# Kernel tuning notes

Measured on AMD Instinct MI355X. Metric: run time of the kernel, lower is better.

## Reference

```python
import jax, jax.numpy as jnp
import numpy as np

DIM, HEADS, WS = 256, 16, 8
B, H, W = 2, 252, 252
BN_EPS = 1e-5


def _rel_index():
    # Same construction as the torch buffer relative_position_index (64,64)
    coords = np.stack(np.meshgrid(np.arange(WS), np.arange(WS), indexing='ij'))
    flat = coords.reshape(2, -1)
    rel = (flat[:, :, None] - flat[:, None, :]).transpose(1, 2, 0).copy()
    rel[..., 0] += WS - 1
    rel[..., 1] += WS - 1
    rel[..., 0] *= 2 * WS - 1
    return jnp.asarray(rel.sum(-1))

REL_IDX = _rel_index()  # (WS*WS, WS*WS) int


def _conv(x, w, pad, groups=1):
    return jax.lax.conv_general_dilated(
        x, w, (1, 1), [(pad[0], pad[0]), (pad[1], pad[1])],
        dimension_numbers=('NCHW', 'OIHW', 'NCHW'), feature_group_count=groups)


def setup_inputs() -> dict:
    key = jax.random.key(0)
    ks = jax.random.split(key, 8)
    s = lambda k, shape, sc: jax.random.normal(k, shape, jnp.float32) * sc
    z = lambda: jnp.zeros((DIM,), jnp.float32)
    return {
        'x': s(ks[0], (B, DIM, H, W), 1.0),
        'w_qkv': s(ks[1], (3 * DIM, DIM, 1, 1), 0.05),
        'rel_bias_table': s(ks[2], ((2 * WS - 1) ** 2, HEADS), 0.02),
        'w_h': s(ks[3], (DIM, DIM, WS, 1), 0.02),
        'b_h': z(),
        'w_v': s(ks[4], (DIM, DIM, 1, WS), 0.02),
        'b_v': z(),
        'w_dw': s(ks[5], (DIM, 1, WS, WS), 0.05),
        'bn_gamma': jnp.ones((DIM,), jnp.float32),
        'bn_beta': z(),
        'bn_mean': z(),
        'bn_var': jnp.ones((DIM,), jnp.float32),
        'w_pw': s(ks[6], (DIM, DIM, 1, 1), 0.05),
    }


def reference(x, w_qkv, rel_bias_table, w_h, b_h, w_v, b_v, w_dw,
              bn_gamma, bn_beta, bn_mean, bn_var, w_pw):
    Bc, C, Hc, Wc = x.shape
    pad_h, pad_w = WS - Hc % WS, WS - Wc % WS
    xp = jnp.pad(x, ((0, 0), (0, 0), (0, pad_h), (0, pad_w)), mode='reflect')
    Hp, Wp = Hc + pad_h, Wc + pad_w
    hh, ww, d = Hp // WS, Wp // WS, C // HEADS

    qkv = _conv(xp, w_qkv, (0, 0))  # (B, 3C, Hp, Wp)
    # b (qkv h d) (hh ws1) (ww ws2) -> qkv (b hh ww) h (ws1 ws2) d
    qkv = qkv.reshape(Bc, 3, HEADS, d, hh, WS, ww, WS)
    qkv = qkv.transpose(1, 0, 4, 6, 2, 5, 7, 3).reshape(3, Bc * hh * ww, HEADS, WS * WS, d)
    q, k, v = qkv[0], qkv[1], qkv[2]

    dots = jnp.einsum('nhid,nhjd->nhij', q, k) * (d ** -0.5)
    bias = rel_bias_table[REL_IDX.reshape(-1)].reshape(WS * WS, WS * WS, HEADS)
    dots = dots + bias.transpose(2, 0, 1)[None]  # (1, h, 64, 64)
    attn = jax.nn.softmax(dots, axis=-1)
    out = jnp.einsum('nhij,nhjd->nhid', attn, v)
    # (b hh ww) h (ws1 ws2) d -> b (h d) (hh ws1) (ww ws2)
    out = out.reshape(Bc, hh, ww, HEADS, WS, WS, d)
    out = out.transpose(0, 3, 6, 1, 4, 2, 5).reshape(Bc, C, Hp, Wp)
    out = out[:, :, :Hc, :Wc]

    p1 = _conv(jnp.pad(out, ((0, 0), (0, 0), (0, 1), (0, 0)), mode='reflect'),
               w_h, (WS // 2 - 1, 0)) + b_h[None, :, None, None]
    p2 = _conv(jnp.pad(out, ((0, 0), (0, 0), (0, 0), (0, 1)), mode='reflect'),
               w_v, (0, WS // 2 - 1)) + b_v[None, :, None, None]
    y = jnp.pad(p1 + p2, ((0, 0), (0, 0), (0, 1), (0, 1)), mode='reflect')
    y = _conv(y, w_dw, ((WS - 1) // 2, (WS - 1) // 2), groups=DIM)  # depthwise
    inv = bn_gamma / jnp.sqrt(bn_var + BN_EPS)
    y = y * inv[None, :, None, None] + (bn_beta - bn_mean * inv)[None, :, None, None]
    y = _conv(y, w_pw, (0, 0))  # pointwise 1x1
    return y[:, :, :Hc, :Wc]
```

## Files before the change

### kernel.cpp

```cpp
#include <hip/hip_runtime.h>
#include <hip/hip_bf16.h>

#define HC 252
#define WC 252
#define CD 256
#define NHEADS 16

#define XP_W 264
#define XP_HW (252*264)
#define XP_CHW (256*252*264)

typedef unsigned short u16;
typedef unsigned int u32;
typedef __attribute__((ext_vector_type(8))) short bf16x8;
typedef __attribute__((ext_vector_type(4))) float f32x4;
typedef __attribute__((ext_vector_type(4))) u32 u32x4;
typedef __attribute__((ext_vector_type(2))) u32 u32x2;

#define XP_BYTES (2u * (unsigned)XP_CHW * 2u)
#define ZP_OFF   XP_BYTES
#define ZP_BYTES 409600u
#define WT_OFF   (ZP_OFF + ZP_BYTES)
#define WT_ELEMS (128*8192)
#define WPW_OFF  (WT_OFF + (unsigned)WT_ELEMS*2u)
#define WPW_ELEMS (8*8192)
#define WQ_OFF   (WPW_OFF + (unsigned)WPW_ELEMS*2u)
#define WQ_ELEMS (768*256)
#define BIAS_OFF (WQ_OFF + (unsigned)WQ_ELEMS*2u)

__device__ __forceinline__ u16 bfu(float f) {
    __hip_bfloat16 h = __float2bfloat16(f);
    return *(reinterpret_cast<u16*>(&h));
}
__device__ __forceinline__ u32 pack2(float a, float b) {
    return (u32)bfu(a) | ((u32)bfu(b) << 16);
}

__global__ __launch_bounds__(256, 2) void attn_mfma(
    const float* __restrict__ x, const u16* __restrict__ WQ,
    const float* __restrict__ BIASF, u16* __restrict__ xp)
{
    __shared__ __align__(16) char smem[73728];

    const int bid = blockIdx.x;
    const int zz = (bid & 7) * 256 + (bid >> 3);
    const int wx = zz & 31, wy = (zz >> 5) & 31, b = zz >> 10;
    const int tid = threadIdx.x;
    const int lane = tid & 63, wid = tid >> 6;
    const int g = lane >> 4, li = lane & 15;

    {
        int ci = tid;
        const float* srcc = x + (size_t)(b * 256 + ci) * (HC * WC);
        #pragma unroll
        for (int r = 0; r < 8; ++r) {
            int h = wy * 8 + r; if (h >= HC) h = 2 * HC - 2 - h;
            const float* src = srcc + h * WC;
            float v[8];
            if (wx == 31) {
                #pragma unroll
                for (int c = 0; c < 8; ++c) {
                    int w = 248 + c; if (w >= WC) w = 2 * WC - 2 - w;
                    v[c] = src[w];
                }
            } else {
                float4 f0 = *(const float4*)(src + wx * 8);
                float4 f1 = *(const float4*)(src + wx * 8 + 4);
                v[0]=f0.x; v[1]=f0.y; v[2]=f0.z; v[3]=f0.w;
                v[4]=f1.x; v[5]=f1.y; v[6]=f1.z; v[7]=f1.w;
            }
            #pragma unroll
            for (int c = 0; c < 8; ++c) {
                int pos = r * 8 + c;
                int byte = pos * 512 + ((ci * 2) ^ ((pos & 7) << 4));
                *(u16*)(smem + byte) = bfu(v[c]);
            }
        }
    }
    __syncthreads();

    const int WB = 32768 + wid * 10240;
    char* Qb = smem + WB;
    char* Kb = smem + WB + 2048;
    char* Vb = smem + WB + 4096;
    char* Pb = smem + WB + 6144;

    const bf16x8 zf = {0,0,0,0,0,0,0,0};

    #pragma unroll 1
    for (int hh = 0; hh < 4; ++hh) {
        const int head = wid * 4 + hh;

        f32x4 acc[3][4];
        #pragma unroll
        for (int p = 0; p < 3; ++p)
            #pragma unroll
            for (int nf = 0; nf < 4; ++nf) acc[p][nf] = (f32x4){0.f,0.f,0.f,0.f};

        for (int ks = 0; ks < 8; ++ks) {
            bf16x8 bx[4];
            #pragma unroll
            for (int nf = 0; nf < 4; ++nf) {
                int pos = 16 * nf + li;
                int byte = pos * 512 + ((ks * 64 + 16 * g) ^ ((pos & 7) << 4));
                bx[nf] = *(const bf16x8*)(smem + byte);
            }
            bf16x8 aw[3];
            #pragma unroll
            for (int p = 0; p < 3; ++p) {
                int o = p * 256 + head * 16 + li;
                aw[p] = *(const bf16x8*)(WQ + o * 256 + ks * 32 + 8 * g);
            }
            __builtin_amdgcn_s_setprio(1);
            #pragma unroll
            for (int p = 0; p < 3; ++p)
                #pragma unroll
                for (int nf = 0; nf < 4; ++nf)
                    acc[p][nf] = __builtin_amdgcn_mfma_f32_16x16x32_bf16(aw[p], bx[nf], acc[p][nf], 0, 0, 0);
            __builtin_amdgcn_s_setprio(0);
        }

        #pragma unroll
        for (int p = 0; p < 3; ++p) {
            if (p < 2) {
                char* base = (p == 0) ? Qb : Kb;
                #pragma unroll
                for (int nf = 0; nf < 4; ++nf) {
                    int pos = 16 * nf + li;
                    u32 lo = pack2(acc[p][nf][0], acc[p][nf][1]);
                    u32 hi = pack2(acc[p][nf][2], acc[p][nf][3]);
                    int byte = pos * 32 + ((8 * g) ^ (((pos >> 2) & 1) << 4));
                    *(u32x2*)(base + byte) = (u32x2){lo, hi};
                }
            } else {
                #pragma unroll
                for (int nf = 0; nf < 4; ++nf) {
                    int pos = 16 * nf + li;
                    #pragma unroll
                    for (int r = 0; r < 4; ++r) {
                        int d = 4 * g + r;
                        int byte = (pos >> 3) * 256 + d * 16 + (pos & 7) * 2;
                        *(u16*)(Vb + byte) = bfu(acc[p][nf][r]);
                    }
                }
            }
        }

        f32x4 s[4][4];
        #pragma unroll
        for (int mf = 0; mf < 4; ++mf)
            #pragma unroll
            for (int nf = 0; nf < 4; ++nf) s[mf][nf] = (f32x4){0.f,0.f,0.f,0.f};
        bf16x8 bk[4];
        #pragma unroll
        for (int nf = 0; nf < 4; ++nf) {
            int pos = 16 * nf + li;
            bk[nf] = (g < 2) ? *(const bf16x8*)(Kb + pos * 32 + ((16 * g) ^ (((pos >> 2) & 1) << 4))) : zf;
        }
        __builtin_amdgcn_s_setprio(1);
        #pragma unroll
        for (int mf = 0; mf < 4; ++mf) {
            int pos = 16 * mf + li;
            bf16x8 aq = (g < 2) ? *(const bf16x8*)(Qb + pos * 32 + ((16 * g) ^ (((pos >> 2) & 1) << 4))) : zf;
            #pragma unroll
            for (int nf = 0; nf < 4; ++nf)
                s[mf][nf] = __builtin_amdgcn_mfma_f32_16x16x32_bf16(aq, bk[nf], s[mf][nf], 0, 0, 0);
        }
        __builtin_amdgcn_s_setprio(0);

        f32x4 e[4][4];
        f32x4 rs[4];
        #pragma unroll
        for (int mf = 0; mf < 4; ++mf) rs[mf] = (f32x4){0.f,0.f,0.f,0.f};
        #pragma unroll
        for (int mf = 0; mf < 4; ++mf)
            #pragma unroll
            for (int nf = 0; nf < 4; ++nf) {
                f32x4 b4 = *(const f32x4*)(BIASF + (((head * 4 + mf) * 4 + nf) * 64 + lane) * 4);
                #pragma unroll
                for (int r = 0; r < 4; ++r) {
                    float ev = __expf(s[mf][nf][r] * 0.25f + b4[r]);
                    e[mf][nf][r] = ev;
                    rs[mf][r] += ev;
                }
            }
        #pragma unroll
        for (int mf = 0; mf < 4; ++mf)
            #pragma unroll
            for (int r = 0; r < 4; ++r) {
                float t = rs[mf][r];
                t += __shfl_xor(t, 1); t += __shfl_xor(t, 2);
                t += __shfl_xor(t, 4); t += __shfl_xor(t, 8);
                rs[mf][r] = t;
            }

        f32x4 o[4];
        #pragma unroll
        for (int mf = 0; mf < 4; ++mf) o[mf] = (f32x4){0.f,0.f,0.f,0.f};
        const bool even = !(lane & 1);
        #pragma unroll
        for (int hf = 0; hf < 2; ++hf) {
            #pragma unroll
            for (int mf = 0; mf < 4; ++mf)
                #pragma unroll
                for (int nfl = 0; nfl < 2; ++nfl) {
                    f32x4 ee = e[mf][2 * hf + nfl];
                    float p0 = __shfl_xor(ee[0], 1), p1 = __shfl_xor(ee[1], 1);
                    float p2 = __shfl_xor(ee[2], 1), p3 = __shfl_xor(ee[3], 1);
                    int jl = 16 * nfl + (li & ~1);
                    u32 w0, w1; int r0;
                    if (even) { w0 = pack2(ee[0], p0); w1 = pack2(ee[1], p1); r0 = 0; }
                    else      { w0 = pack2(p2, ee[2]); w1 = pack2(p3, ee[3]); r0 = 2; }
                    int i0 = 16 * mf + 4 * g + r0, i1 = i0 + 1;
                    *(u32*)(Pb + i0 * 64 + ((2 * jl) ^ ((i0 & 3) << 4))) = w0;
                    *(u32*)(Pb + i1 * 64 + ((2 * jl) ^ ((i1 & 3) << 4))) = w1;
                }
            bf16x8 bv = *(const bf16x8*)(Vb + (4 * hf + g) * 256 + li * 16);
            __builtin_amdgcn_s_setprio(1);
            #pragma unroll
            for (int mf = 0; mf < 4; ++mf) {
                int i = 16 * mf + li;
                bf16x8 ap = *(const bf16x8*)(Pb + i * 64 + ((16 * g) ^ ((i & 3) << 4)));
                o[mf] = __builtin_amdgcn_mfma_f32_16x16x32_bf16(ap, bv, o[mf], 0, 0, 0);
            }
            __builtin_amdgcn_s_setprio(0);
        }

        #pragma unroll
        for (int mf = 0; mf < 4; ++mf) {
            int h = wy * 8 + 2 * mf + (g >> 1);
            int wbase = wx * 8 + 4 * (g & 1);
            if (h < HC && wbase < WC) {
                float v0 = o[mf][0] / rs[mf][0], v1 = o[mf][1] / rs[mf][1];
                float v2 = o[mf][2] / rs[mf][2], v3 = o[mf][3] / rs[mf][3];
                size_t idx = ((size_t)(b * 256 + head * 16 + li) * HC + h) * XP_W + wbase + 4;
                *(u32x2*)(xp + idx) = (u32x2){pack2(v0, v1), pack2(v2, v3)};
            }
        }
    }
}

__global__ __launch_bounds__(256) void wprep_kernel(
    const float* __restrict__ wh, const float* __restrict__ wv,
    const float* __restrict__ wpw, const float* __restrict__ wqkv,
    const float* __restrict__ btab, u16* __restrict__ wsu)
{
    int i = blockIdx.x * 256 + threadIdx.x;
    u16* WT = wsu + WT_OFF / 2;
    u16* WP = wsu + WPW_OFF / 2;
    u16* ZP = wsu + ZP_OFF / 2;
    u16* WQp = wsu + WQ_OFF / 2;
    float* BF = (float*)(wsu + BIAS_OFF / 2);
    if (i < WT_ELEMS) {
        int j = i & 7, co = (i >> 3) & 255, kb = (i >> 11) & 3, s = i >> 13;
        float v = (s < 64) ? wh[co * 2048 + s * 32 + kb * 8 + j]
                           : wv[co * 2048 + (s - 64) * 32 + kb * 8 + j];
        WT[i] = bfu(v);
    } else if (i < WT_ELEMS + WPW_ELEMS) {
        int i2 = i - WT_ELEMS;
        int j = i2 & 7, co = (i2 >> 3) & 255, kb = (i2 >> 11) & 3, s = i2 >> 13;
        WP[i2] = bfu(wpw[co * 256 + s * 32 + kb * 8 + j]);
    } else if (i < WT_ELEMS + WPW_ELEMS + (int)(ZP_BYTES / 2)) {
        ZP[i - WT_ELEMS - WPW_ELEMS] = 0;
    } else if (i < WT_ELEMS + WPW_ELEMS + (int)(ZP_BYTES / 2) + WQ_ELEMS) {
        int i4 = i - WT_ELEMS - WPW_ELEMS - (int)(ZP_BYTES / 2);
        WQp[i4] = bfu(wqkv[i4]);
    } else {
        int i5 = i - WT_ELEMS - WPW_ELEMS - (int)(ZP_BYTES / 2) - WQ_ELEMS;
        if (i5 < 16384) {
            int lane = i5 & 63, nf = (i5 >> 6) & 3, mf = (i5 >> 8) & 3, head = i5 >> 10;
            int gg = lane >> 4, ll = lane & 15;
            #pragma unroll
            for (int r = 0; r < 4; ++r) {
                int row = 16 * mf + 4 * gg + r;
                int col = 16 * nf + ll;
                int dy = (row >> 3) - (col >> 3) + 7;
                int dx = (row & 7) - (col & 7) + 7;
                BF[i5 * 4 + r] = btab[(dy * 15 + dx) * NHEADS + head];
            }
        }
    }
}

__global__ __launch_bounds__(256) void halo_kernel(u16* __restrict__ xp)
{
    int i = blockIdx.x * 256 + threadIdx.x;
    if (i >= 129024 * 12) return;
    int row = i / 12, c = i % 12;
    int wp = (c < 4) ? c : 252 + c;
    u16 v = 0;
    if (wp == 256) v = xp[row * XP_W + 254];
    xp[row * XP_W + wp] = v;
}

__global__ __launch_bounds__(512, 2) void sepconv_mfma(
    const u16* __restrict__ xp, const u16* __restrict__ WT,
    const u16* __restrict__ ZP,
    const float* __restrict__ b_h, const float* __restrict__ b_v,
    float* __restrict__ P)
{
    __shared__ u16 As[2][8192];
    __shared__ u16 Bs[2][256 * 36];

    const int bid = blockIdx.x;
    const int zz = (bid & 7) * 63 + (bid >> 3);
    const int h = zz % HC, b = zz / HC;
    const int tid = threadIdx.x;
    const int lane = tid & 63, wid = tid >> 6;
    const int wr = wid >> 2, wc = wid & 3;
    const int cq = lane & 15, kb = lane >> 4;

    const int wl2 = (tid & 127) * 2;
    const int oc = tid >> 7;

    const u16* hcur[8];
    int hstep[8];
    #pragma unroll
    for (int t = 0; t < 8; ++t) {
        int j = h + t - 3;
        bool valid = (j >= 0 && j <= 252);
        int jr = (j == 252) ? 250 : j;
        hcur[t] = valid ? (xp + (size_t)b * XP_CHW + (size_t)jr * XP_W) : ZP;
        hstep[t] = valid ? 4 * XP_HW : 0;
    }
    const u16* vbase = xp + (size_t)b * XP_CHW + (size_t)h * XP_W;
    const int hvoff = oc * XP_HW + wl2 + 4;

    const int bw0 = wl2 * 36 + oc * 8;
    const int bw1 = bw0 + 36;

    f32x4 acc[8][4];
    #pragma unroll
    for (int m = 0; m < 8; ++m)
        #pragma unroll
        for (int n = 0; n < 4; ++n) acc[m][n] = (f32x4){0.f, 0.f, 0.f, 0.f};

    u32x4 rA[2];
    u32 rB[8];

    int aw0, aw1;
    {
        int c0 = tid, c1 = 512 + tid;
        aw0 = ((c0 >> 8) * 256 + ((c0 & 255) ^ (((c0 >> 8) & 3) << 1))) * 8;
        aw1 = ((c1 >> 8) * 256 + ((c1 & 255) ^ (((c1 >> 8) & 3) << 1))) * 8;
    }

    rA[0] = *(const u32x4*)(WT + (size_t)tid * 8);
    rA[1] = *(const u32x4*)(WT + (size_t)(512 + tid) * 8);
    #pragma unroll
    for (int t = 0; t < 8; ++t)
        rB[t] = *(const u32*)(hcur[t] + hvoff);
    *(u32x4*)&As[0][aw0] = rA[0];
    *(u32x4*)&As[0][aw1] = rA[1];
    {
        union { bf16x8 v; u32 u[4]; } p0, p1;
        #pragma unroll
        for (int q = 0; q < 4; ++q) {
            p0.u[q] = __builtin_amdgcn_perm(rB[2 * q + 1], rB[2 * q], 0x05040100u);
            p1.u[q] = __builtin_amdgcn_perm(rB[2 * q + 1], rB[2 * q], 0x07060302u);
        }
        *(bf16x8*)&Bs[0][bw0] = p0.v;
        *(bf16x8*)&Bs[0][bw1] = p1.v;
    }

    for (int s = 0; s < 128; ++s) {
        const int cur = s & 1;
        const int s1 = s + 1;
        const bool hph1 = (s1 < 64);
        if (s1 < 128) {
            rA[0] = *(const u32x4*)(WT + (size_t)s1 * 8192 + (size_t)tid * 8);
            rA[1] = *(const u32x4*)(WT + (size_t)s1 * 8192 + (size_t)(512 + tid) * 8);
            if (hph1) {
                #pragma unroll
                for (int t = 0; t < 8; ++t) hcur[t] += hstep[t];
                #pragma unroll
                for (int t = 0; t < 8; ++t)
                    rB[t] = *(const u32*)(hcur[t] + hvoff);
            } else {
                int off = ((s1 - 64) * 4 + oc) * XP_HW + wl2;
                #pragma unroll
                for (int l = 0; l < 6; ++l)
                    rB[l] = *(const u32*)(vbase + off + 2 * l);
            }
        }
        __syncthreads();

        bf16x8 af[8], bfr[4];
        #pragma unroll
        for (int m = 0; m < 8; ++m) {
            int row = wr * 128 + m * 16 + cq;
            af[m] = *(const bf16x8*)&As[cur][(kb * 256 + (row ^ (kb << 1))) * 8];
        }
        #pragma unroll
        for (int n = 0; n < 4; ++n)
            bfr[n] = *(const bf16x8*)&Bs[cur][(wc * 64 + n * 16 + cq) * 36 + kb * 8];
        #pragma unroll
        for (int m = 0; m < 8; ++m)
            #pragma unroll
            for (int n = 0; n < 4; ++n)
                acc[m][n] = __builtin_amdgcn_mfma_f32_16x16x32_bf16(af[m], bfr[n], acc[m][n], 0, 0, 0);

        if (s1 < 128) {
            const int nxt = cur ^ 1;
            *(u32x4*)&As[nxt][aw0] = rA[0];
            *(u32x4*)&As[nxt][aw1] = rA[1];
            union { bf16x8 v; u32 u[4]; } p0, p1;
            if (hph1) {
                #pragma unroll
                for (int q = 0; q < 4; ++q) {
                    p0.u[q] = __builtin_amdgcn_perm(rB[2 * q + 1], rB[2 * q], 0x05040100u);
                    p1.u[q] = __builtin_amdgcn_perm(rB[2 * q + 1], rB[2 * q], 0x07060302u);
                }
            } else {
                #pragma unroll
                for (int q = 0; q < 4; ++q)
                    p0.u[q] = __builtin_amdgcn_alignbit(rB[q + 1], rB[q], 16);
                p1.u[0] = rB[1]; p1.u[1] = rB[2];
                p1.u[2] = rB[3]; p1.u[3] = rB[4];
            }
            *(bf16x8*)&Bs[nxt][bw0] = p0.v;
            *(bf16x8*)&Bs[nxt][bw1] = p1.v;
        }
    }

    const int rq = lane >> 4, cc = lane & 15;
    #pragma unroll
    for (int m = 0; m < 8; ++m) {
        int cgb = wr * 128 + m * 16 + rq * 4;
        float bias[4];
        #pragma unroll
        for (int rr = 0; rr < 4; ++rr) bias[rr] = b_h[cgb + rr] + b_v[cgb + rr];
        #pragma unroll
        for (int n = 0; n < 4; ++n) {
            int wg = wc * 64 + n * 16 + cc;
            if (wg < WC) {
                #pragma unroll
                for (int rr = 0; rr < 4; ++rr)
                    P[((size_t)(b * CD + cgb + rr) * HC + h) * WC + wg] = acc[m][n][rr] + bias[rr];
            }
        }
    }
}

__global__ __launch_bounds__(256) void dwbn_kernel(
    const float* __restrict__ P, const float* __restrict__ w_dw,
    const float* __restrict__ gamma, const float* __restrict__ beta,
    const float* __restrict__ mean, const float* __restrict__ var,
    __hip_bfloat16* __restrict__ Yb)
{
    __shared__ float ps[15][42];
    __shared__ float wd[64];
    const int bw = blockIdx.x, bh = blockIdx.y, bz = blockIdx.z;
    const int b = bz >> 8, c = bz & 255;
    const int h0 = bh * 8, w0 = bw * 32;
    const int tid = threadIdx.x;
    if (tid < 64) wd[tid] = w_dw[c * 64 + tid];
    for (int it = 0; it < 3; ++it) {
        int flat = tid + it * 256;
        if (flat < 630) {
            int row = flat / 42, col = flat % 42;
            int j = h0 - 3 + row, wcol = w0 - 3 + col;
            float v = 0.f;
            if (j >= 0 && j <= HC && wcol >= 0 && wcol <= WC) {
                int jr = (j == HC) ? (HC - 2) : j;
                int wr2 = (wcol == WC) ? (WC - 2) : wcol;
                v = P[((b * CD + c) * HC + jr) * WC + wr2];
            }
            ps[row][col] = v;
        }
    }
    __syncthreads();
    const int r = tid >> 5, cc = tid & 31;
    const int h = h0 + r, w = w0 + cc;
    if (h < HC && w < WC) {
        float s = 0.f;
        #pragma unroll
        for (int u = 0; u < 8; ++u)
            #pragma unroll
            for (int v2 = 0; v2 < 8; ++v2)
                s += wd[u * 8 + v2] * ps[r + u][cc + v2];
        const float inv = gamma[c] * rsqrtf(var[c] + 1e-5f);
        Yb[((b * CD + c) * HC + h) * WC + w] = __float2bfloat16(s * inv + (beta[c] - mean[c] * inv));
    }
}

__global__ __launch_bounds__(512, 2) void pw_mfma(
    const u16* __restrict__ Y, const u16* __restrict__ WP,
    float* __restrict__ O)
{
    __shared__ u16 As[2][8192];
    __shared__ u16 Bs[2][256 * 36];

    const int bid = blockIdx.x;
    const int zz = (bid & 7) * 63 + (bid >> 3);
    const int h = zz % HC, b = zz / HC;
    const int tid = threadIdx.x;
    const int lane = tid & 63, wid = tid >> 6;
    const int wr = wid >> 2, wc = wid & 3;
    const int cq = lane & 15, kb = lane >> 4;

    const int wl2 = (tid & 127) * 2;
    const int oc = tid >> 7;

    const u16* yb = Y + ((size_t)(b * 256 + oc * 8) * HC + h) * WC + wl2;

    const int bw0 = wl2 * 36 + oc * 8;
    const int bw1 = bw0 + 36;

    f32x4 acc[8][4];
    #pragma unroll
    for (int m = 0; m < 8; ++m)
        #pragma unroll
        for (int n = 0; n < 4; ++n) acc[m][n] = (f32x4){0.f, 0.f, 0.f, 0.f};

    u32x4 rA[2];
    u32 rB[8];

    int aw0, aw1;
    {
        int c0 = tid, c1 = 512 + tid;
        aw0 = ((c0 >> 8) * 256 + ((c0 & 255) ^ (((c0 >> 8) & 3) << 1))) * 8;
        aw1 = ((c1 >> 8) * 256 + ((c1 & 255) ^ (((c1 >> 8) & 3) << 1))) * 8;
    }

    rA[0] = *(const u32x4*)(WP + (size_t)tid * 8);
    rA[1] = *(const u32x4*)(WP + (size_t)(512 + tid) * 8);
    #pragma unroll
    for (int j = 0; j < 8; ++j)
        rB[j] = *(const u32*)(yb + (size_t)j * (HC * WC));
    *(u32x4*)&As[0][aw0] = rA[0];
    *(u32x4*)&As[0][aw1] = rA[1];
    {
        union { bf16x8 v; u32 u[4]; } p0, p1;
        #pragma unroll
        for (int q = 0; q < 4; ++q) {
            p0.u[q] = __builtin_amdgcn_perm(rB[2 * q + 1], rB[2 * q], 0x05040100u);
            p1.u[q] = __builtin_amdgcn_perm(rB[2 * q + 1], rB[2 * q], 0x07060302u);
        }
        *(bf16x8*)&Bs[0][bw0] = p0.v;
        *(bf16x8*)&Bs[0][bw1] = p1.v;
    }

    for (int s = 0; s < 8; ++s) {
        const int cur = s & 1;
        const int s1 = s + 1;
        if (s1 < 8) {
            rA[0] = *(const u32x4*)(WP + (size_t)s1 * 8192 + (size_t)tid * 8);
            rA[1] = *(const u32x4*)(WP + (size_t)s1 * 8192 + (size_t)(512 + tid) * 8);
            #pragma unroll
            for (int j = 0; j < 8; ++j)
                rB[j] = *(const u32*)(yb + (size_t)(s1 * 32 + j) * (HC * WC));
        }
        __syncthreads();

        bf16x8 af[8], bfr[4];
        #pragma unroll
        for (int m = 0; m < 8; ++m) {
            int row = wr * 128 + m * 16 + cq;
            af[m] = *(const bf16x8*)&As[cur][(kb * 256 + (row ^ (kb << 1))) * 8];
        }
        #pragma unroll
        for (int n = 0; n < 4; ++n)
            bfr[n] = *(const bf16x8*)&Bs[cur][(wc * 64 + n * 16 + cq) * 36 + kb * 8];
        #pragma unroll
        for (int m = 0; m < 8; ++m)
            #pragma unroll
            for (int n = 0; n < 4; ++n)
                acc[m][n] = __builtin_amdgcn_mfma_f32_16x16x32_bf16(af[m], bfr[n], acc[m][n], 0, 0, 0);

        if (s1 < 8) {
            const int nxt = cur ^ 1;
            *(u32x4*)&As[nxt][aw0] = rA[0];
            *(u32x4*)&As[nxt][aw1] = rA[1];
            union { bf16x8 v; u32 u[4]; } p0, p1;
            #pragma unroll
            for (int q = 0; q < 4; ++q) {
                p0.u[q] = __builtin_amdgcn_perm(rB[2 * q + 1], rB[2 * q], 0x05040100u);
                p1.u[q] = __builtin_amdgcn_perm(rB[2 * q + 1], rB[2 * q], 0x07060302u);
            }
            *(bf16x8*)&Bs[nxt][bw0] = p0.v;
            *(bf16x8*)&Bs[nxt][bw1] = p1.v;
        }
    }

    const int rq = lane >> 4, cc = lane & 15;
    #pragma unroll
    for (int m = 0; m < 8; ++m) {
        int cgb = wr * 128 + m * 16 + rq * 4;
        #pragma unroll
        for (int n = 0; n < 4; ++n) {
            int wg = wc * 64 + n * 16 + cc;
            if (wg < WC) {
                #pragma unroll
                for (int rr = 0; rr < 4; ++rr)
                    O[((size_t)(b * CD + cgb + rr) * HC + h) * WC + wg] = acc[m][n][rr];
            }
        }
    }
}

extern "C" void kernel_launch(void* const* d_in, const int* in_sizes, int n_in,
                              void* d_out, int out_size, void* d_ws, size_t ws_size,
                              hipStream_t stream)
{
    const float* x      = (const float*)d_in[0];
    const float* w_qkv  = (const float*)d_in[1];
    const float* bias_t = (const float*)d_in[2];
    const float* w_h    = (const float*)d_in[3];
    const float* b_h    = (const float*)d_in[4];
    const float* w_v    = (const float*)d_in[5];
    const float* b_v    = (const float*)d_in[6];
    const float* w_dw   = (const float*)d_in[7];
    const float* bn_g   = (const float*)d_in[8];
    const float* bn_b   = (const float*)d_in[9];
    const float* bn_m   = (const float*)d_in[10];
    const float* bn_v   = (const float*)d_in[11];
    const float* w_pw   = (const float*)d_in[12];
    float* out = (float*)d_out;

    u16* wsu = (u16*)d_ws;
    const u16* XPu = wsu;
    const u16* ZPu = wsu + ZP_OFF / 2;
    const u16* WTu = wsu + WT_OFF / 2;
    const u16* WPu = wsu + WPW_OFF / 2;
    const u16* WQu = wsu + WQ_OFF / 2;
    const float* BFu = (const float*)(wsu + BIAS_OFF / 2);

    wprep_kernel<<<5984, 256, 0, stream>>>(w_h, w_v, w_pw, w_qkv, bias_t, wsu);
    attn_mfma<<<2048, 256, 0, stream>>>(x, WQu, BFu, wsu);
    halo_kernel<<<6048, 256, 0, stream>>>(wsu);
    sepconv_mfma<<<504, 512, 0, stream>>>(XPu, WTu, ZPu, b_h, b_v, out);
    dwbn_kernel<<<dim3(8, 32, 512), 256, 0, stream>>>(out, w_dw, bn_g, bn_b, bn_m, bn_v,
                                                      (__hip_bfloat16*)d_ws);
    pw_mfma<<<504, 512, 0, stream>>>(wsu, WPu, out);
}
```

Before: 677.1 us.

## Use direct global-to-LDS weight loads and store sepconv output as bf16

```diff
diff --git a/kernel.cpp b/kernel.cpp
--- a/kernel.cpp
+++ b/kernel.cpp
@@ -34,6 +34,9 @@
 }
 __device__ __forceinline__ u32 pack2(float a, float b) {
     return (u32)bfu(a) | ((u32)bfu(b) << 16);
+}
+__device__ __forceinline__ float bf2f(u16 v) {
+    union { u32 u; float f; } cv; cv.u = ((u32)v) << 16; return cv.f;
 }
 
 __global__ __launch_bounds__(256, 2) void attn_mfma(
@@ -252,13 +255,17 @@
     u16* WQp = wsu + WQ_OFF / 2;
     float* BF = (float*)(wsu + BIAS_OFF / 2);
     if (i < WT_ELEMS) {
-        int j = i & 7, co = (i >> 3) & 255, kb = (i >> 11) & 3, s = i >> 13;
+        int j = i & 7, l = (i >> 3) & 1023, s = i >> 13;
+        int kb = (l >> 8) & 3;
+        int co = (l & 255) ^ (kb << 1);
         float v = (s < 64) ? wh[co * 2048 + s * 32 + kb * 8 + j]
                            : wv[co * 2048 + (s - 64) * 32 + kb * 8 + j];
         WT[i] = bfu(v);
     } else if (i < WT_ELEMS + WPW_ELEMS) {
         int i2 = i - WT_ELEMS;
-        int j = i2 & 7, co = (i2 >> 3) & 255, kb = (i2 >> 11) & 3, s = i2 >> 13;
+        int j = i2 & 7, l = (i2 >> 3) & 1023, s = i2 >> 13;
+        int kb = (l >> 8) & 3;
+        int co = (l & 255) ^ (kb << 1);
         WP[i2] = bfu(wpw[co * 256 + s * 32 + kb * 8 + j]);
     } else if (i < WT_ELEMS + WPW_ELEMS + (int)(ZP_BYTES / 2)) {
         ZP[i - WT_ELEMS - WPW_ELEMS] = 0;
@@ -297,10 +304,10 @@
     const u16* __restrict__ xp, const u16* __restrict__ WT,
     const u16* __restrict__ ZP,
     const float* __restrict__ b_h, const float* __restrict__ b_v,
-    float* __restrict__ P)
+    u16* __restrict__ P)
 {
-    __shared__ u16 As[2][8192];
-    __shared__ u16 Bs[2][256 * 36];
+    __shared__ __align__(16) u16 As[2][8192];
+    __shared__ __align__(16) u16 Bs[2][256 * 36];
 
     const int bid = blockIdx.x;
     const int zz = (bid & 7) * 63 + (bid >> 3);
@@ -335,93 +342,86 @@
         #pragma unroll
         for (int n = 0; n < 4; ++n) acc[m][n] = (f32x4){0.f, 0.f, 0.f, 0.f};
 
-    u32x4 rA[2];
     u32 rB[8];
 
-    int aw0, aw1;
-    {
-        int c0 = tid, c1 = 512 + tid;
-        aw0 = ((c0 >> 8) * 256 + ((c0 & 255) ^ (((c0 >> 8) & 3) << 1))) * 8;
-        aw1 = ((c1 >> 8) * 256 + ((c1 & 255) ^ (((c1 >> 8) & 3) << 1))) * 8;
-    }
-
-    rA[0] = *(const u32x4*)(WT + (size_t)tid * 8);
-    rA[1] = *(const u32x4*)(WT + (size_t)(512 + tid) * 8);
-    #pragma unroll
-    for (int t = 0; t < 8; ++t)
-        rB[t] = *(const u32*)(hcur[t] + hvoff);
-    *(u32x4*)&As[0][aw0] = rA[0];
-    *(u32x4*)&As[0][aw1] = rA[1];
-    {
-        union { bf16x8 v; u32 u[4]; } p0, p1;
-        #pragma unroll
-        for (int q = 0; q < 4; ++q) {
-            p0.u[q] = __builtin_amdgcn_perm(rB[2 * q + 1], rB[2 * q], 0x05040100u);
-            p1.u[q] = __builtin_amdgcn_perm(rB[2 * q + 1], rB[2 * q], 0x07060302u);
-        }
-        *(bf16x8*)&Bs[0][bw0] = p0.v;
-        *(bf16x8*)&Bs[0][bw1] = p1.v;
-    }
-
+#define SC_GLA(t, buf)                                                         \
+    if ((t) < 128) {                                                           \
+        __builtin_amdgcn_global_load_lds(                                      \
+            (const u32*)(WT + (size_t)(t) * 8192 + (size_t)tid * 8),           \
+            (u32*)&As[buf][(size_t)tid * 8], 16, 0, 0);                        \
+        __builtin_amdgcn_global_load_lds(                                      \
+            (const u32*)(WT + (size_t)(t) * 8192 + (size_t)(512 + tid) * 8),   \
+            (u32*)&As[buf][(size_t)(512 + tid) * 8], 16, 0, 0);                \
+    }
+
+#define SC_ADV()                                                               \
+    { _Pragma("unroll") for (int tt = 0; tt < 8; ++tt) hcur[tt] += hstep[tt]; }
+
+#define SC_LOADB(t)                                                            \
+    if ((t) < 128) {                                                           \
+        if ((t) < 64) {                                                        \
+            _Pragma("unroll") for (int tt = 0; tt < 8; ++tt)                   \
+                rB[tt] = *(const u32*)(hcur[tt] + hvoff);                      \
+        } else {                                                               \
+            int off_ = (((t) - 64) * 4 + oc) * XP_HW + wl2;                    \
+            _Pragma("unroll") for (int l = 0; l < 6; ++l)                      \
+                rB[l] = *(const u32*)(vbase + off_ + 2 * l);                   \
+        }                                                                      \
+    }
+
+#define SC_WRITEB(t, buf)                                                      \
+    if ((t) < 128) {                                                           \
+        union { bf16x8 v; u32 u[4]; } p0_, p1_;                                \
+        if ((t) < 64) {                                                        \
+            _Pragma("unroll") for (int q = 0; q < 4; ++q) {                    \
+                p0_.u[q] = __builtin_amdgcn_perm(rB[2*q+1], rB[2*q], 0x05040100u); \
+                p1_.u[q] = __builtin_amdgcn_perm(rB[2*q+1], rB[2*q], 0x07060302u); \
+            }                                                                  \
+        } else {                                                               \
+            _Pragma("unroll") for (int q = 0; q < 4; ++q)                      \
+                p0_.u[q] = __builtin_amdgcn_alignbit(rB[q+1], rB[q], 16);      \
+            p1_.u[0] = rB[1]; p1_.u[1] = rB[2]; p1_.u[2] = rB[3]; p1_.u[3] = rB[4]; \
+        }                                                                      \
+        *(bf16x8*)&Bs[buf][bw0] = p0_.v;                                       \
+        *(bf16x8*)&Bs[buf][bw1] = p1_.v;                                       \
+    }
+
+    SC_GLA(0, 0)
+    SC_LOADB(0)
+    SC_WRITEB(0, 0)
+
+    #pragma unroll 1
     for (int s = 0; s < 128; ++s) {
         const int cur = s & 1;
+        const int nxt = cur ^ 1;
         const int s1 = s + 1;
-        const bool hph1 = (s1 < 64);
-        if (s1 < 128) {
-            rA[0] = *(const u32x4*)(WT + (size_t)s1 * 8192 + (size_t)tid * 8);
-            rA[1] = *(const u32x4*)(WT + (size_t)s1 * 8192 + (size_t)(512 + tid) * 8);
-            if (hph1) {
-                #pragma unroll
-                for (int t = 0; t < 8; ++t) hcur[t] += hstep[t];
-                #pragma unroll
-                for (int t = 0; t < 8; ++t)
-                    rB[t] = *(const u32*)(hcur[t] + hvoff);
-            } else {
-                int off = ((s1 - 64) * 4 + oc) * XP_HW + wl2;
-                #pragma unroll
-                for (int l = 0; l < 6; ++l)
-                    rB[l] = *(const u32*)(vbase + off + 2 * l);
-            }
-        }
         __syncthreads();
-
-        bf16x8 af[8], bfr[4];
-        #pragma unroll
-        for (int m = 0; m < 8; ++m) {
-            int row = wr * 128 + m * 16 + cq;
-            af[m] = *(const bf16x8*)&As[cur][(kb * 256 + (row ^ (kb << 1))) * 8];
-        }
-        #pragma unroll
-        for (int n = 0; n < 4; ++n)
-            bfr[n] = *(const bf16x8*)&Bs[cur][(wc * 64 + n * 16 + cq) * 36 + kb * 8];
-        #pragma unroll
-        for (int m = 0; m < 8; ++m)
+        if (s1 < 64) { SC_ADV() }
+        SC_LOADB(s1)
+        SC_GLA(s1, nxt)
+        {
+            bf16x8 af[8], bfr[4];
+            #pragma unroll
+            for (int m = 0; m < 8; ++m) {
+                int row = wr * 128 + m * 16 + cq;
+                af[m] = *(const bf16x8*)&As[cur][(kb * 256 + (row ^ (kb << 1))) * 8];
+            }
             #pragma unroll
             for (int n = 0; n < 4; ++n)
-                acc[m][n] = __builtin_amdgcn_mfma_f32_16x16x32_bf16(af[m], bfr[n], acc[m][n], 0, 0, 0);
-
-        if (s1 < 128) {
-            const int nxt = cur ^ 1;
-            *(u32x4*)&As[nxt][aw0] = rA[0];
-            *(u32x4*)&As[nxt][aw1] = rA[1];
-            union { bf16x8 v; u32 u[4]; } p0, p1;
-            if (hph1) {
-                #pragma unroll
-                for (int q = 0; q < 4; ++q) {
-                    p0.u[q] = __builtin_amdgcn_perm(rB[2 * q + 1], rB[2 * q], 0x05040100u);
-                    p1.u[q] = __builtin_amdgcn_perm(rB[2 * q + 1], rB[2 * q], 0x07060302u);
-                }
-            } else {
-                #pragma unroll
-                for (int q = 0; q < 4; ++q)
-                    p0.u[q] = __builtin_amdgcn_alignbit(rB[q + 1], rB[q], 16);
-                p1.u[0] = rB[1]; p1.u[1] = rB[2];
-                p1.u[2] = rB[3]; p1.u[3] = rB[4];
-            }
-            *(bf16x8*)&Bs[nxt][bw0] = p0.v;
-            *(bf16x8*)&Bs[nxt][bw1] = p1.v;
-        }
-    }
+                bfr[n] = *(const bf16x8*)&Bs[cur][(wc * 64 + n * 16 + cq) * 36 + kb * 8];
+            #pragma unroll
+            for (int m = 0; m < 8; ++m)
+                #pragma unroll
+                for (int n = 0; n < 4; ++n)
+                    acc[m][n] = __builtin_amdgcn_mfma_f32_16x16x32_bf16(af[m], bfr[n], acc[m][n], 0, 0, 0);
+        }
+        SC_WRITEB(s1, nxt)
+    }
+
+#undef SC_GLA
+#undef SC_ADV
+#undef SC_LOADB
+#undef SC_WRITEB
 
     const int rq = lane >> 4, cc = lane & 15;
     #pragma unroll
@@ -436,14 +436,14 @@
             if (wg < WC) {
                 #pragma unroll
                 for (int rr = 0; rr < 4; ++rr)
-                    P[((size_t)(b * CD + cgb + rr) * HC + h) * WC + wg] = acc[m][n][rr] + bias[rr];
+                    P[((size_t)(b * CD + cgb + rr) * HC + h) * WC + wg] = bfu(acc[m][n][rr] + bias[rr]);
             }
         }
     }
 }
 
 __global__ __launch_bounds__(256) void dwbn_kernel(
-    const float* __restrict__ P, const float* __restrict__ w_dw,
+    const u16* __restrict__ P, const float* __restrict__ w_dw,
     const float* __restrict__ gamma, const float* __restrict__ beta,
     const float* __restrict__ mean, const float* __restrict__ var,
     __hip_bfloat16* __restrict__ Yb)
@@ -464,7 +464,7 @@
             if (j >= 0 && j <= HC && wcol >= 0 && wcol <= WC) {
                 int jr = (j == HC) ? (HC - 2) : j;
                 int wr2 = (wcol == WC) ? (WC - 2) : wcol;
-                v = P[((b * CD + c) * HC + jr) * WC + wr2];
+                v = bf2f(P[((size_t)(b * CD + c) * HC + jr) * WC + wr2]);
             }
             ps[row][col] = v;
         }
@@ -488,8 +488,8 @@
     const u16* __restrict__ Y, const u16* __restrict__ WP,
     float* __restrict__ O)
 {
-    __shared__ u16 As[2][8192];
-    __shared__ u16 Bs[2][256 * 36];
+    __shared__ __align__(16) u16 As[2][8192];
+    __shared__ __align__(16) u16 Bs[2][256 * 36];
 
     const int bid = blockIdx.x;
     const int zz = (bid & 7) * 63 + (bid >> 3);
@@ -513,75 +513,69 @@
         #pragma unroll
         for (int n = 0; n < 4; ++n) acc[m][n] = (f32x4){0.f, 0.f, 0.f, 0.f};
 
-    u32x4 rA[2];
     u32 rB[8];
 
-    int aw0, aw1;
-    {
-        int c0 = tid, c1 = 512 + tid;
-        aw0 = ((c0 >> 8) * 256 + ((c0 & 255) ^ (((c0 >> 8) & 3) << 1))) * 8;
-        aw1 = ((c1 >> 8) * 256 + ((c1 & 255) ^ (((c1 >> 8) & 3) << 1))) * 8;
-    }
-
-    rA[0] = *(const u32x4*)(WP + (size_t)tid * 8);
-    rA[1] = *(const u32x4*)(WP + (size_t)(512 + tid) * 8);
-    #pragma unroll
-    for (int j = 0; j < 8; ++j)
-        rB[j] = *(const u32*)(yb + (size_t)j * (HC * WC));
-    *(u32x4*)&As[0][aw0] = rA[0];
-    *(u32x4*)&As[0][aw1] = rA[1];
-    {
-        union { bf16x8 v; u32 u[4]; } p0, p1;
-        #pragma unroll
-        for (int q = 0; q < 4; ++q) {
-            p0.u[q] = __builtin_amdgcn_perm(rB[2 * q + 1], rB[2 * q], 0x05040100u);
-            p1.u[q] = __builtin_amdgcn_perm(rB[2 * q + 1], rB[2 * q], 0x07060302u);
-        }
-        *(bf16x8*)&Bs[0][bw0] = p0.v;
-        *(bf16x8*)&Bs[0][bw1] = p1.v;
-    }
-
+#define PW_GLA(t, buf)                                                         \
+    if ((t) < 8) {                                                             \
+        __builtin_amdgcn_global_load_lds(                                      \
+            (const u32*)(WP + (size_t)(t) * 8192 + (size_t)tid * 8),           \
+            (u32*)&As[buf][(size_t)tid * 8], 16, 0, 0);                        \
+        __builtin_amdgcn_global_load_lds(                                      \
+            (const u32*)(WP + (size_t)(t) * 8192 + (size_t)(512 + tid) * 8),   \
+            (u32*)&As[buf][(size_t)(512 + tid) * 8], 16, 0, 0);                \
+    }
+
+#define PW_LOADB(t)                                                            \
+    if ((t) < 8) {                                                             \
+        _Pragma("unroll") for (int j = 0; j < 8; ++j)                          \
+            rB[j] = *(const u32*)(yb + (size_t)((t) * 32 + j) * (HC * WC));    \
+    }
+
+#define PW_WRITEB(t, buf)                                                      \
+    if ((t) < 8) {                                                             \
+        union { bf16x8 v; u32 u[4]; } p0_, p1_;                                \
+        _Pragma("unroll") for (int q = 0; q < 4; ++q) {                        \
+            p0_.u[q] = __builtin_amdgcn_perm(rB[2*q+1], rB[2*q], 0x05040100u); \
+            p1_.u[q] = __builtin_amdgcn_perm(rB[2*q+1], rB[2*q], 0x07060302u); \
+        }                                                                      \
+        *(bf16x8*)&Bs[buf][bw0] = p0_.v;                                       \
+        *(bf16x8*)&Bs[buf][bw1] = p1_.v;                                       \
+    }
+
+    PW_GLA(0, 0)
+    PW_LOADB(0)
+    PW_WRITEB(0, 0)
+
+    #pragma unroll 1
     for (int s = 0; s < 8; ++s) {
         const int cur = s & 1;
+        const int nxt = cur ^ 1;
         const int s1 = s + 1;
-        if (s1 < 8) {
-            rA[0] = *(const u32x4*)(WP + (size_t)s1 * 8192 + (size_t)tid * 8);
-            rA[1] = *(const u32x4*)(WP + (size_t)s1 * 8192 + (size_t)(512 + tid) * 8);
-            #pragma unroll
-            for (int j = 0; j < 8; ++j)
-                rB[j] = *(const u32*)(yb + (size_t)(s1 * 32 + j) * (HC * WC));
-        }
         __syncthreads();
-
-        bf16x8 af[8], bfr[4];
-        #pragma unroll
-        for (int m = 0; m < 8; ++m) {
-            int row = wr * 128 + m * 16 + cq;
-            af[m] = *(const bf16x8*)&As[cur][(kb * 256 + (row ^ (kb << 1))) * 8];
-        }
-        #pragma unroll
-        for (int n = 0; n < 4; ++n)
-            bfr[n] = *(const bf16x8*)&Bs[cur][(wc * 64 + n * 16 + cq) * 36 + kb * 8];
-        #pragma unroll
-        for (int m = 0; m < 8; ++m)
+        PW_LOADB(s1)
+        PW_GLA(s1, nxt)
+        {
+            bf16x8 af[8], bfr[4];
+            #pragma unroll
+            for (int m = 0; m < 8; ++m) {
+                int row = wr * 128 + m * 16 + cq;
+                af[m] = *(const bf16x8*)&As[cur][(kb * 256 + (row ^ (kb << 1))) * 8];
+            }
             #pragma unroll
             for (int n = 0; n < 4; ++n)
-                acc[m][n] = __builtin_amdgcn_mfma_f32_16x16x32_bf16(af[m], bfr[n], acc[m][n], 0, 0, 0);
-
-        if (s1 < 8) {
-            const int nxt = cur ^ 1;
-            *(u32x4*)&As[nxt][aw0] = rA[0];
-            *(u32x4*)&As[nxt][aw1] = rA[1];
-            union { bf16x8 v; u32 u[4]; } p0, p1;
-            #pragma unroll
-            for (int q = 0; q < 4; ++q) {
-                p0.u[q] = __builtin_amdgcn_perm(rB[2 * q + 1], rB[2 * q], 0x05040100u);
-                p1.u[q] = __builtin_amdgcn_perm(rB[2 * q + 1], rB[2 * q], 0x07060302u);
-            }
-            *(bf16x8*)&Bs[nxt][bw0] = p0.v;
-            *(bf16x8*)&Bs[nxt][bw1] = p1.v;
-        }
-    }
+                bfr[n] = *(const bf16x8*)&Bs[cur][(wc * 64 + n * 16 + cq) * 36 + kb * 8];
+            #pragma unroll
+            for (int m = 0; m < 8; ++m)
+                #pragma unroll
+                for (int n = 0; n < 4; ++n)
+                    acc[m][n] = __builtin_amdgcn_mfma_f32_16x16x32_bf16(af[m], bfr[n], acc[m][n], 0, 0, 0);
+        }
+        PW_WRITEB(s1, nxt)
+    }
+
+#undef PW_GLA
+#undef PW_LOADB
+#undef PW_WRITEB
 
     const int rq = lane >> 4, cc = lane & 15;
     #pragma unroll
@@ -629,8 +623,8 @@
     wprep_kernel<<<5984, 256, 0, stream>>>(w_h, w_v, w_pw, w_qkv, bias_t, wsu);
     attn_mfma<<<2048, 256, 0, stream>>>(x, WQu, BFu, wsu);
     halo_kernel<<<6048, 256, 0, stream>>>(wsu);
-    sepconv_mfma<<<504, 512, 0, stream>>>(XPu, WTu, ZPu, b_h, b_v, out);
-    dwbn_kernel<<<dim3(8, 32, 512), 256, 0, stream>>>(out, w_dw, bn_g, bn_b, bn_m, bn_v,
-                                                      (__hip_bfloat16*)d_ws);
+    sepconv_mfma<<<504, 512, 0, stream>>>(XPu, WTu, ZPu, b_h, b_v, (u16*)d_out);
+    dwbn_kernel<<<dim3(8, 32, 512), 256, 0, stream>>>((const u16*)d_out, w_dw, bn_g, bn_b,
+                                                      bn_m, bn_v, (__hip_bfloat16*)d_ws);
     pw_mfma<<<504, 512, 0, stream>>>(wsu, WPu, out);
 }
```

Result: slower. 765.4 us (+13.0%).
